# Performance work log

Measured on AMD Instinct MI355X. Metric: run time of the kernel, lower is better.

The kernel has to match this reference:

```python
import jax, jax.numpy as jnp
import numpy as np

BETA = 1.0
ALPHA = 0.5


def setup_inputs() -> dict:
    key = jax.random.key(0)
    k1, k2, k3 = jax.random.split(key, 3)
    B, N1, N2 = 512, 256, 32768
    v = jax.random.normal(k1, (B, N1), dtype=jnp.float32)
    mask = jax.random.uniform(k2, (B, N1), dtype=jnp.float32)
    Mem = jax.random.normal(k3, (N2, N1), dtype=jnp.float32)  # kernel [N2, N1] (trailing 1 squeezed)
    return {"v": v, "mask": mask, "Mem": Mem}


def reference(v, mask, Mem):
    # Squared L2 distance d2[i, b] = ||Mem[i] - v[b]||^2, computed without the
    # [N2, N1, B] diff tensor via the expansion ||m||^2 - 2 m.v + ||v||^2.
    m2 = jnp.sum(Mem * Mem, axis=1)            # [N2]
    v2 = jnp.sum(v * v, axis=1)                # [B]
    cross = jnp.einsum('nd,bd->nb', Mem, v)    # [N2, B]
    d2 = m2[:, None] - 2.0 * cross + v2[None, :]
    # Gaussian-kernel weights over the N2 stored patterns (softmax == exp/sum).
    w = jax.nn.softmax(-0.5 * BETA * d2, axis=0)  # [N2, B]
    # update[b] = sum_i w[i,b] * (Mem[i] - v[b]) = (w^T Mem)[b] - v[b]
    update = jnp.einsum('nb,nd->bd', w, Mem) - v   # [B, N1]
    return v + ALPHA * update * mask
```

## Files before the change

### kernel.cpp

```cpp
#include <hip/hip_runtime.h>
#include <hip/hip_bf16.h>
#include <stdint.h>

typedef float  f32x4  __attribute__((ext_vector_type(4)));
typedef float  f32x16 __attribute__((ext_vector_type(16)));
typedef _Float16 half8 __attribute__((ext_vector_type(8)));
typedef unsigned int uint32;

#define N1 256
#define N2T 32768
#define BQ 512
#define KT 32
#define TILE_B 16384

#define RA_OFF 0
#define MT_OFF 32768
#define LDS_BYTES 65536

union H4 { _Float16 h[4]; unsigned short s[4]; uint2 u2; };

#define GLD_LDS(gp, lp) __builtin_amdgcn_global_load_lds( \
    (const __attribute__((address_space(1))) void*)(gp), \
    (__attribute__((address_space(3))) void*)(lp), 16, 0, 0)

__global__ __launch_bounds__(256) void mhn_prep_k(
    const float* __restrict__ Mem, _Float16* __restrict__ MemA,
    _Float16* __restrict__ MemT, float* __restrict__ m2g)
{
  const int t   = blockIdx.x;
  const int tid = threadIdx.x;
  const int a    = tid >> 4;
  const int dblk = tid & 15;
  const int r0i  = 32*t + 2*a;

  const float* p0 = Mem + (size_t)r0i*N1 + dblk*16;
  const float* p1 = p0 + N1;
  float4 x0[4], x1[4];
  #pragma unroll
  for (int i=0;i<4;i++){ x0[i] = *(const float4*)(p0+4*i); x1[i] = *(const float4*)(p1+4*i); }

  float s0=0.f, s1=0.f;
  H4 h0[4], h1[4];
  #pragma unroll
  for (int i=0;i<4;i++){
    s0 += x0[i].x*x0[i].x + x0[i].y*x0[i].y + x0[i].z*x0[i].z + x0[i].w*x0[i].w;
    s1 += x1[i].x*x1[i].x + x1[i].y*x1[i].y + x1[i].z*x1[i].z + x1[i].w*x1[i].w;
    h0[i].h[0]=(_Float16)x0[i].x; h0[i].h[1]=(_Float16)x0[i].y; h0[i].h[2]=(_Float16)x0[i].z; h0[i].h[3]=(_Float16)x0[i].w;
    h1[i].h[0]=(_Float16)x1[i].x; h1[i].h[1]=(_Float16)x1[i].y; h1[i].h[2]=(_Float16)x1[i].z; h1[i].h[3]=(_Float16)x1[i].w;
  }

  char* bA = (char*)MemA + (size_t)t*TILE_B;
  {
    const int e0 = (2*a)&7, e1 = (2*a+1)&7;
    uint4 wv;
    wv.x=h0[0].u2.x; wv.y=h0[0].u2.y; wv.z=h0[1].u2.x; wv.w=h0[1].u2.y;
    *(uint4*)(bA + (2*a)*512   + (((2*dblk  )^e0)<<4)) = wv;
    wv.x=h0[2].u2.x; wv.y=h0[2].u2.y; wv.z=h0[3].u2.x; wv.w=h0[3].u2.y;
    *(uint4*)(bA + (2*a)*512   + (((2*dblk+1)^e0)<<4)) = wv;
    wv.x=h1[0].u2.x; wv.y=h1[0].u2.y; wv.z=h1[1].u2.x; wv.w=h1[1].u2.y;
    *(uint4*)(bA + (2*a+1)*512 + (((2*dblk  )^e1)<<4)) = wv;
    wv.x=h1[2].u2.x; wv.y=h1[2].u2.y; wv.z=h1[3].u2.x; wv.w=h1[3].u2.y;
    *(uint4*)(bA + (2*a+1)*512 + (((2*dblk+1)^e1)<<4)) = wv;
  }

  char* bT = (char*)MemT + (size_t)t*TILE_B;
  #pragma unroll
  for (int i=0;i<4;i++){
    #pragma unroll
    for (int j=0;j<4;j++){
      const int d = dblk*16 + 4*i + j;
      const uint32 pk = (uint32)h0[i].s[j] | ((uint32)h1[i].s[j] << 16);
      *(uint32*)(bT + d*64 + ((((a>>2) ^ ((d>>1)&3)))<<4) + ((a&3)<<2)) = pk;
    }
  }

  s0 += __shfl_xor(s0,1); s0 += __shfl_xor(s0,2); s0 += __shfl_xor(s0,4); s0 += __shfl_xor(s0,8);
  s1 += __shfl_xor(s1,1); s1 += __shfl_xor(s1,2); s1 += __shfl_xor(s1,4); s1 += __shfl_xor(s1,8);
  if (dblk == 0){ m2g[r0i] = -0.5f*s0; m2g[r0i+1] = -0.5f*s1; }
}

__global__ __launch_bounds__(256, 2) void mhn_flash_k(
    const _Float16* __restrict__ MemA, const _Float16* __restrict__ MemT,
    const float* __restrict__ m2g, const float* __restrict__ v,
    __hip_bfloat16* __restrict__ Opart, float* __restrict__ mpart,
    float* __restrict__ lpart, int CK, int nt)
{
  __shared__ __align__(16) char lds[LDS_BYTES];

  const int tid = threadIdx.x;
  const int w   = tid >> 6;
  const int l   = tid & 63;
  const int row = l & 31;
  const int hi  = l >> 5;

  const int nwg = gridDim.x;
  const int bid = blockIdx.x;
  const int s_  = (bid & 7) * (nwg >> 3) + (bid >> 3);
  const int c   = s_ >> 2;
  const int qb  = s_ & 3;

  const uint32 dmaL = (uint32)(w*4096 + l*16);
  const char* gA = (const char*)MemA + (size_t)(c*(CK>>5))*TILE_B + dmaL;
  const char* gT = (const char*)MemT + (size_t)(c*(CK>>5))*TILE_B + dmaL;
  char* const dA0 = lds + RA_OFF + dmaL;
  char* const dT0 = lds + MT_OFF + dmaL;

  #pragma unroll
  for (int i=0;i<4;i++){
    GLD_LDS(gA + i*1024, dA0 + i*1024);
    GLD_LDS(gT + i*1024, dT0 + i*1024);
  }
  gA += TILE_B; gT += TILE_B;

  half8 v8[16];
  const int q0 = qb*128 + w*32;
  {
    const float* vp = v + (size_t)(q0 + row)*N1 + 8*hi;
    #pragma unroll
    for (int s=0;s<16;s++){
      const float4 a = *(const float4*)(vp + 16*s);
      const float4 b = *(const float4*)(vp + 16*s + 4);
      half8 hv;
      hv[0]=(_Float16)a.x; hv[1]=(_Float16)a.y; hv[2]=(_Float16)a.z; hv[3]=(_Float16)a.w;
      hv[4]=(_Float16)b.x; hv[5]=(_Float16)b.y; hv[6]=(_Float16)b.z; hv[7]=(_Float16)b.w;
      v8[s]=hv;
    }
  }

  float mrun = -INFINITY, lrun = 0.f;
  f32x16 oacc[8];
  #pragma unroll
  for (int b=0;b<8;b++) oacc[b] = (f32x16)(0.f);

  const int e7 = row & 7;
  const uint32 qkB = (uint32)(row*512 + ((hi ^ (e7 & 1)) << 4) + ((e7 >> 1) << 5));
  const int sd = (row >> 1) & 3;
  const uint32 pvB = (uint32)(row*64 + ((hi ^ (sd & 1)) << 4) + ((sd >> 1) << 5));

  const float* m2p = m2g + c*CK + 8*0 + 4*hi;

  __syncthreads();

  for (int tt=0; tt<nt; ++tt){
    const uint32 bufO = (uint32)(tt & 1)*TILE_B;
    const bool pf = (tt+1 < nt);
    if (pf){
      const char* sA = gA; const char* sT = gT;
      char* dA = dA0 + (bufO ^ TILE_B);
      char* dT = dT0 + (bufO ^ TILE_B);
      #pragma unroll
      for (int i=0;i<4;i++){
        GLD_LDS(sA + i*1024, dA + i*1024);
        GLD_LDS(sT + i*1024, dT + i*1024);
      }
      gA += TILE_B; gT += TILE_B;
    }

    f32x4 m2v[4];
    #pragma unroll
    for (int b=0;b<4;b++) m2v[b] = *(const f32x4*)(m2p + 8*b);

    const char* ra = lds + RA_OFF + bufO;
    f32x16 S = (f32x16)(0.f);
    __builtin_amdgcn_s_setprio(1);
    #pragma unroll
    for (int s=0;s<16;s++){
      const half8 a = *(const half8*)(ra + (qkB ^ (uint32)(s<<5)));
      S = __builtin_amdgcn_mfma_f32_32x32x16_f16(a, v8[s], S, 0,0,0);
    }
    __builtin_amdgcn_s_setprio(0);

    float p[16];
    #pragma unroll
    for (int r=0;r<16;r++) p[r] = S[r] + m2v[r>>2][r&3];

    float t01=fmaxf(p[0],p[1]),   t23=fmaxf(p[2],p[3]),   t45=fmaxf(p[4],p[5]),   t67=fmaxf(p[6],p[7]);
    float t89=fmaxf(p[8],p[9]),   tAB=fmaxf(p[10],p[11]), tCD=fmaxf(p[12],p[13]), tEF=fmaxf(p[14],p[15]);
    float q03=fmaxf(t01,t23), q47=fmaxf(t45,t67), q8B=fmaxf(t89,tAB), qCF=fmaxf(tCD,tEF);
    float tm = fmaxf(fmaxf(q03,q47), fmaxf(q8B,qCF));
    tm = fmaxf(tm, __shfl_xor(tm, 32));
    if (__any(tm > mrun + 8.0f)){
      const float nm = fmaxf(mrun, tm);
      const float sc = __expf(mrun - nm);
      lrun *= sc; mrun = nm;
      #pragma unroll
      for (int b=0;b<8;b++) oacc[b] *= sc;
    }
    #pragma unroll
    for (int r=0;r<16;r++) p[r] = __expf(p[r] - mrun);

    uint32 D[8];
    #pragma unroll
    for (int i=0;i<8;i++){
      union { __fp16 h2 __attribute__((ext_vector_type(2))); uint32 u; } cv;
      cv.h2 = __builtin_amdgcn_cvt_pkrtz(p[2*i], p[2*i+1]);
      D[i] = cv.u;
    }
    uint32 wq[8];
    {
      const uint32 tD0 = (uint32)__shfl_xor((int)D[0], 32);
      const uint32 tD1 = (uint32)__shfl_xor((int)D[1], 32);
      const uint32 tD2 = (uint32)__shfl_xor((int)D[2], 32);
      const uint32 tD3 = (uint32)__shfl_xor((int)D[3], 32);
      const uint32 tD4 = (uint32)__shfl_xor((int)D[4], 32);
      const uint32 tD5 = (uint32)__shfl_xor((int)D[5], 32);
      const uint32 tD6 = (uint32)__shfl_xor((int)D[6], 32);
      const uint32 tD7 = (uint32)__shfl_xor((int)D[7], 32);
      const bool lo = (hi == 0);
      wq[0] = lo ? D[0] : tD2;  wq[1] = lo ? D[1] : tD3;
      wq[2] = lo ? tD0 : D[2];  wq[3] = lo ? tD1 : D[3];
      wq[4] = lo ? D[4] : tD6;  wq[5] = lo ? D[5] : tD7;
      wq[6] = lo ? tD4 : D[6];  wq[7] = lo ? tD5 : D[7];
    }
    union { uint32 u[4]; half8 h; } pb1, pb2;
    pb1.u[0]=wq[0]; pb1.u[1]=wq[1]; pb1.u[2]=wq[2]; pb1.u[3]=wq[3];
    pb2.u[0]=wq[4]; pb2.u[1]=wq[5]; pb2.u[2]=wq[6]; pb2.u[3]=wq[7];

    const char* mtb = lds + MT_OFF + bufO;
    const char* a1 = (const char*)(mtb + pvB);
    const char* a2 = (const char*)(mtb + (pvB ^ 32u));
    __builtin_amdgcn_s_setprio(1);
    #pragma unroll
    for (int b=0;b<8;b++){
      const half8 A1 = *(const half8*)(a1 + b*2048);
      oacc[b] = __builtin_amdgcn_mfma_f32_32x32x16_f16(A1, pb1.h, oacc[b], 0,0,0);
      const half8 A2 = *(const half8*)(a2 + b*2048);
      oacc[b] = __builtin_amdgcn_mfma_f32_32x32x16_f16(A2, pb2.h, oacc[b], 0,0,0);
    }
    __builtin_amdgcn_s_setprio(0);

    float s01=p[0]+p[1],   s23=p[2]+p[3],   s45=p[4]+p[5],   s67=p[6]+p[7];
    float s89=p[8]+p[9],   sAB=p[10]+p[11], sCD=p[12]+p[13], sEF=p[14]+p[15];
    float u03=s01+s23, u47=s45+s67, u8B=s89+sAB, uCF=sCD+sEF;
    float ps = (u03+u47) + (u8B+uCF);
    ps += __shfl_xor(ps, 32); lrun += ps;

    m2p += KT;
    __syncthreads();
  }

  {
    __hip_bfloat16* Op = Opart + (size_t)c*N1*BQ + (q0 + row);
    #pragma unroll
    for (int b=0;b<8;b++){
      #pragma unroll
      for (int r=0;r<16;r++){
        const int d = 32*b + (r&3) + 8*(r>>2) + 4*hi;
        Op[(size_t)d*BQ] = __float2bfloat16(oacc[b][r]);
      }
    }
    if (hi == 0){
      mpart[(size_t)c*BQ + q0 + row] = mrun;
      lpart[(size_t)c*BQ + q0 + row] = lrun;
    }
  }
}

__global__ __launch_bounds__(128) void mhn_wprep_k(
    const float* __restrict__ mpart, const float* __restrict__ lpart,
    float* __restrict__ W, float* __restrict__ invL, int nchunk)
{
  __shared__ float sred[2];
  const int q = blockIdx.x;
  const int c = threadIdx.x;
  const int l = c & 63, wv = c >> 6;

  const float m = (c < nchunk) ? mpart[(size_t)c*BQ + q] : -INFINITY;
  const float lv = (c < nchunk) ? lpart[(size_t)c*BQ + q] : 0.f;

  float r = m;
  r = fmaxf(r, __shfl_xor(r,1));  r = fmaxf(r, __shfl_xor(r,2));
  r = fmaxf(r, __shfl_xor(r,4));  r = fmaxf(r, __shfl_xor(r,8));
  r = fmaxf(r, __shfl_xor(r,16)); r = fmaxf(r, __shfl_xor(r,32));
  if (l == 0) sred[wv] = r;
  __syncthreads();
  const float M = fmaxf(sred[0], sred[1]);
  __syncthreads();

  const float e = __expf(m - M);
  float s = lv * e;
  s += __shfl_xor(s,1);  s += __shfl_xor(s,2);
  s += __shfl_xor(s,4);  s += __shfl_xor(s,8);
  s += __shfl_xor(s,16); s += __shfl_xor(s,32);
  if (l == 0) sred[wv] = s;
  __syncthreads();

  if (c < nchunk) W[(size_t)c*BQ + q] = e;
  if (c == 0) invL[q] = 1.0f / (sred[0] + sred[1]);
}

__global__ __launch_bounds__(256) void mhn_wsum_k(
    const float* __restrict__ v, const float* __restrict__ mask,
    const __hip_bfloat16* __restrict__ Opart, const float* __restrict__ W,
    const float* __restrict__ invL, float* __restrict__ out, int nchunk)
{
  const int g = blockIdx.x*256 + threadIdx.x;
  const int q = g & (BQ-1);
  const int d = g >> 9;

  const __hip_bfloat16* op = Opart + (size_t)d*BQ + q;
  const float* wp = W + q;
  float acc = 0.f;
  #pragma unroll 8
  for (int c2=0; c2<nchunk; c2++){
    acc += __bfloat162float(op[(size_t)c2*N1*BQ]) * wp[(size_t)c2*BQ];
  }
  const float vv = v[(size_t)q*N1 + d], mk = mask[(size_t)q*N1 + d];
  out[(size_t)q*N1 + d] = vv + 0.5f*(acc*invL[q] - vv)*mk;
}

extern "C" void kernel_launch(void* const* d_in, const int* in_sizes, int n_in,
                              void* d_out, int out_size, void* d_ws, size_t ws_size,
                              hipStream_t stream)
{
  (void)in_sizes; (void)n_in; (void)out_size;
  const float* v    = (const float*)d_in[0];
  const float* mask = (const float*)d_in[1];
  const float* Mem  = (const float*)d_in[2];
  float* out = (float*)d_out;

  const size_t fixedB   = (size_t)N2T*N1*2*2 + (size_t)N2T*4 + (size_t)BQ*4;
  const size_t perChunk = (size_t)BQ*N1*2 + (size_t)BQ*12;
  int nchunk = 128;
  while (nchunk > 4 && fixedB + (size_t)nchunk*perChunk > ws_size) nchunk >>= 1;

  char* wsb = (char*)d_ws;
  _Float16* MemA = (_Float16*)wsb;
  _Float16* MemT = (_Float16*)(wsb + (size_t)N2T*N1*2);
  float*    m2g  = (float*)(wsb + (size_t)N2T*N1*4);
  float*    invL = (float*)(wsb + (size_t)N2T*N1*4 + (size_t)N2T*4);
  char* pb = wsb + fixedB;
  __hip_bfloat16* Opart = (__hip_bfloat16*)pb;
  float* mpart = (float*)(pb + (size_t)nchunk*BQ*N1*2);
  float* lpart = mpart + (size_t)nchunk*BQ;
  float* W     = lpart + (size_t)nchunk*BQ;

  const int CK = N2T / nchunk;
  const int nt = CK / KT;

  mhn_prep_k<<<dim3(N2T/KT), dim3(256), 0, stream>>>(Mem, MemA, MemT, m2g);
  mhn_flash_k<<<dim3(4*nchunk), dim3(256), 0, stream>>>(MemA, MemT, m2g, v, Opart, mpart, lpart, CK, nt);
  mhn_wprep_k<<<dim3(BQ), dim3(128), 0, stream>>>(mpart, lpart, W, invL, nchunk);
  mhn_wsum_k<<<dim3((N1*BQ)/256), dim3(256), 0, stream>>>(v, mask, Opart, W, invL, out, nchunk);
}
```

Measured before the change: 69.40 us.

## Fuse softmax combine kernels and prefetch LDS operands in flash MFMA loops

Merges the weight-prep and weighted-sum kernels into one combine kernel. Each block recomputes the per-query max and normaliser for 64 queries, keeps the chunk weights in shared memory and writes coalesced output through an LDS transpose. This removes one launch and the W/invL round trip through global memory. In the flash kernel, LDS A-operand reads for both MFMA loops are software-prefetched into registers ahead of use to hide LDS latency, at the cost of extra VGPRs. The combine kernel redundantly rereads mpart/lpart in every d-block.

```diff
diff --git a/kernel.cpp b/kernel.cpp
--- a/kernel.cpp
+++ b/kernel.cpp
@@ -137,7 +137,7 @@
   const int sd = (row >> 1) & 3;
   const uint32 pvB = (uint32)(row*64 + ((hi ^ (sd & 1)) << 4) + ((sd >> 1) << 5));
 
-  const float* m2p = m2g + c*CK + 8*0 + 4*hi;
+  const float* m2p = m2g + c*CK + 4*hi;
 
   __syncthreads();
 
@@ -161,11 +161,15 @@
     for (int b=0;b<4;b++) m2v[b] = *(const f32x4*)(m2p + 8*b);
 
     const char* ra = lds + RA_OFF + bufO;
+    half8 aq[4];
+    #pragma unroll
+    for (int i=0;i<4;i++) aq[i] = *(const half8*)(ra + (qkB ^ (uint32)(i<<5)));
     f32x16 S = (f32x16)(0.f);
     __builtin_amdgcn_s_setprio(1);
     #pragma unroll
     for (int s=0;s<16;s++){
-      const half8 a = *(const half8*)(ra + (qkB ^ (uint32)(s<<5)));
+      const half8 a = aq[s&3];
+      if (s < 12) aq[s&3] = *(const half8*)(ra + (qkB ^ (uint32)((s+4)<<5)));
       S = __builtin_amdgcn_mfma_f32_32x32x16_f16(a, v8[s], S, 0,0,0);
     }
     __builtin_amdgcn_s_setprio(0);
@@ -219,12 +223,19 @@
     const char* mtb = lds + MT_OFF + bufO;
     const char* a1 = (const char*)(mtb + pvB);
     const char* a2 = (const char*)(mtb + (pvB ^ 32u));
+    half8 r1[2], r2[2];
+    r1[0] = *(const half8*)(a1);
+    r2[0] = *(const half8*)(a2);
     __builtin_amdgcn_s_setprio(1);
     #pragma unroll
     for (int b=0;b<8;b++){
-      const half8 A1 = *(const half8*)(a1 + b*2048);
+      const half8 A1 = r1[b&1];
+      const half8 A2 = r2[b&1];
+      if (b < 7){
+        r1[(b+1)&1] = *(const half8*)(a1 + (b+1)*2048);
+        r2[(b+1)&1] = *(const half8*)(a2 + (b+1)*2048);
+      }
       oacc[b] = __builtin_amdgcn_mfma_f32_32x32x16_f16(A1, pb1.h, oacc[b], 0,0,0);
-      const half8 A2 = *(const half8*)(a2 + b*2048);
       oacc[b] = __builtin_amdgcn_mfma_f32_32x32x16_f16(A2, pb2.h, oacc[b], 0,0,0);
     }
     __builtin_amdgcn_s_setprio(0);
@@ -256,57 +267,58 @@
   }
 }
 
-__global__ __launch_bounds__(128) void mhn_wprep_k(
-    const float* __restrict__ mpart, const float* __restrict__ lpart,
-    float* __restrict__ W, float* __restrict__ invL, int nchunk)
+__global__ __launch_bounds__(256) void mhn_combine_k(
+    const float* __restrict__ v, const float* __restrict__ mask,
+    const __hip_bfloat16* __restrict__ Opart, const float* __restrict__ mpart,
+    const float* __restrict__ lpart, float* __restrict__ out, int nchunk)
 {
-  __shared__ float sred[2];
-  const int q = blockIdx.x;
-  const int c = threadIdx.x;
-  const int l = c & 63, wv = c >> 6;
-
-  const float m = (c < nchunk) ? mpart[(size_t)c*BQ + q] : -INFINITY;
-  const float lv = (c < nchunk) ? lpart[(size_t)c*BQ + q] : 0.f;
-
-  float r = m;
-  r = fmaxf(r, __shfl_xor(r,1));  r = fmaxf(r, __shfl_xor(r,2));
-  r = fmaxf(r, __shfl_xor(r,4));  r = fmaxf(r, __shfl_xor(r,8));
-  r = fmaxf(r, __shfl_xor(r,16)); r = fmaxf(r, __shfl_xor(r,32));
-  if (l == 0) sred[wv] = r;
-  __syncthreads();
-  const float M = fmaxf(sred[0], sred[1]);
-  __syncthreads();
-
-  const float e = __expf(m - M);
-  float s = lv * e;
-  s += __shfl_xor(s,1);  s += __shfl_xor(s,2);
-  s += __shfl_xor(s,4);  s += __shfl_xor(s,8);
-  s += __shfl_xor(s,16); s += __shfl_xor(s,32);
-  if (l == 0) sred[wv] = s;
-  __syncthreads();
-
-  if (c < nchunk) W[(size_t)c*BQ + q] = e;
-  if (c == 0) invL[q] = 1.0f / (sred[0] + sred[1]);
-}
-
-__global__ __launch_bounds__(256) void mhn_wsum_k(
-    const float* __restrict__ v, const float* __restrict__ mask,
-    const __hip_bfloat16* __restrict__ Opart, const float* __restrict__ W,
-    const float* __restrict__ invL, float* __restrict__ out, int nchunk)
-{
-  const int g = blockIdx.x*256 + threadIdx.x;
-  const int q = g & (BQ-1);
-  const int d = g >> 9;
-
-  const __hip_bfloat16* op = Opart + (size_t)d*BQ + q;
-  const float* wp = W + q;
+  __shared__ float Wl[128][64];
+  __shared__ float red[4][64];
+  __shared__ float Mq[64];
+  __shared__ float iLq[64];
+  __shared__ float T[256];
+
+  const int bid = blockIdx.x;
+  const int q0  = (bid & 7) * 64;
+  const int d0  = (bid >> 3) * 4;
+  const int t   = threadIdx.x;
+  const int q   = t & 63;
+  const int cg  = t >> 6;
+  const int nc4 = nchunk >> 2;
+
+  float mx = -INFINITY;
+  for (int k=0;k<nc4;k++)
+    mx = fmaxf(mx, mpart[(size_t)(cg*nc4+k)*BQ + q0 + q]);
+  red[cg][q] = mx;
+  __syncthreads();
+  if (t < 64) Mq[t] = fmaxf(fmaxf(red[0][t],red[1][t]), fmaxf(red[2][t],red[3][t]));
+  __syncthreads();
+  const float M = Mq[q];
+  float ls = 0.f;
+  for (int k=0;k<nc4;k++){
+    const int cc = cg*nc4 + k;
+    const float e = __expf(mpart[(size_t)cc*BQ + q0 + q] - M);
+    Wl[cc][q] = e;
+    ls += lpart[(size_t)cc*BQ + q0 + q] * e;
+  }
+  red[cg][q] = ls;
+  __syncthreads();
+  if (t < 64) iLq[t] = 1.0f / (((red[0][t]+red[1][t]) + (red[2][t]+red[3][t])));
+  __syncthreads();
+
+  const int dl = t >> 6;
+  const __hip_bfloat16* op = Opart + (size_t)(d0+dl)*BQ + q0 + q;
   float acc = 0.f;
   #pragma unroll 8
-  for (int c2=0; c2<nchunk; c2++){
-    acc += __bfloat162float(op[(size_t)c2*N1*BQ]) * wp[(size_t)c2*BQ];
-  }
-  const float vv = v[(size_t)q*N1 + d], mk = mask[(size_t)q*N1 + d];
-  out[(size_t)q*N1 + d] = vv + 0.5f*(acc*invL[q] - vv)*mk;
+  for (int c2=0; c2<nchunk; c2++)
+    acc += __bfloat162float(op[(size_t)c2*N1*BQ]) * Wl[c2][q];
+  T[q*4 + dl] = acc * iLq[q];
+  __syncthreads();
+
+  const int q2 = t >> 2, d2 = t & 3;
+  const size_t oi = (size_t)(q0+q2)*N1 + d0 + d2;
+  const float vv = v[oi], mk = mask[oi];
+  out[oi] = vv + 0.5f*(T[t] - vv)*mk;
 }
 
 extern "C" void kernel_launch(void* const* d_in, const int* in_sizes, int n_in,
@@ -319,8 +331,8 @@
   const float* Mem  = (const float*)d_in[2];
   float* out = (float*)d_out;
 
-  const size_t fixedB   = (size_t)N2T*N1*2*2 + (size_t)N2T*4 + (size_t)BQ*4;
-  const size_t perChunk = (size_t)BQ*N1*2 + (size_t)BQ*12;
+  const size_t fixedB   = (size_t)N2T*N1*2*2 + (size_t)N2T*4;
+  const size_t perChunk = (size_t)BQ*N1*2 + (size_t)BQ*8;
   int nchunk = 128;
   while (nchunk > 4 && fixedB + (size_t)nchunk*perChunk > ws_size) nchunk >>= 1;
 
@@ -328,18 +340,15 @@
   _Float16* MemA = (_Float16*)wsb;
   _Float16* MemT = (_Float16*)(wsb + (size_t)N2T*N1*2);
   float*    m2g  = (float*)(wsb + (size_t)N2T*N1*4);
-  float*    invL = (float*)(wsb + (size_t)N2T*N1*4 + (size_t)N2T*4);
   char* pb = wsb + fixedB;
   __hip_bfloat16* Opart = (__hip_bfloat16*)pb;
   float* mpart = (float*)(pb + (size_t)nchunk*BQ*N1*2);
   float* lpart = mpart + (size_t)nchunk*BQ;
-  float* W     = lpart + (size_t)nchunk*BQ;
 
   const int CK = N2T / nchunk;
   const int nt = CK / KT;
 
   mhn_prep_k<<<dim3(N2T/KT), dim3(256), 0, stream>>>(Mem, MemA, MemT, m2g);
   mhn_flash_k<<<dim3(4*nchunk), dim3(256), 0, stream>>>(MemA, MemT, m2g, v, Opart, mpart, lpart, CK, nt);
-  mhn_wprep_k<<<dim3(BQ), dim3(128), 0, stream>>>(mpart, lpart, W, invL, nchunk);
-  mhn_wsum_k<<<dim3((N1*BQ)/256), dim3(256), 0, stream>>>(v, mask, Opart, W, invL, out, nchunk);
+  mhn_combine_k<<<dim3(512), dim3(256), 0, stream>>>(v, mask, Opart, mpart, lpart, out, nchunk);
 }
```

Measured after the change: 73.41 us. 1.06x slower.

## Process two query tiles per wave to reuse each LDS Mem fragment twice

Applied to the files above, without the earlier changes.

Each wave now handles 64 queries as two 32-query sub-tiles, so every half8 fragment read from LDS feeds two MFMAs in both the score and the accumulation GEMMs. The grid halves, so each workgroup covers 256 queries and the global/LDS traffic for Mem tiles is amortised over twice the queries. The cost is doubled accumulator and v-fragment registers, which forces launch bounds down to one block per SIMD-group. The setprio hints are also dropped. Lower occupancy and fewer workgroups may hurt latency hiding.

```diff
diff --git a/kernel.cpp b/kernel.cpp
--- a/kernel.cpp
+++ b/kernel.cpp
@@ -79,7 +79,7 @@
   if (dblk == 0){ m2g[r0i] = -0.5f*s0; m2g[r0i+1] = -0.5f*s1; }
 }
 
-__global__ __launch_bounds__(256, 2) void mhn_flash_k(
+__global__ __launch_bounds__(256, 1) void mhn_flash_k(
     const _Float16* __restrict__ MemA, const _Float16* __restrict__ MemT,
     const float* __restrict__ m2g, const float* __restrict__ v,
     __hip_bfloat16* __restrict__ Opart, float* __restrict__ mpart,
@@ -96,8 +96,8 @@
   const int nwg = gridDim.x;
   const int bid = blockIdx.x;
   const int s_  = (bid & 7) * (nwg >> 3) + (bid >> 3);
-  const int c   = s_ >> 2;
-  const int qb  = s_ & 3;
+  const int c   = s_ >> 1;
+  const int qh  = s_ & 1;
 
   const uint32 dmaL = (uint32)(w*4096 + l*16);
   const char* gA = (const char*)MemA + (size_t)(c*(CK>>5))*TILE_B + dmaL;
@@ -112,32 +112,38 @@
   }
   gA += TILE_B; gT += TILE_B;
 
-  half8 v8[16];
-  const int q0 = qb*128 + w*32;
+  half8 v8a[16], v8b[16];
+  const int q0 = qh*256 + w*64;
   {
-    const float* vp = v + (size_t)(q0 + row)*N1 + 8*hi;
+    const float* vpa = v + (size_t)(q0 + row)*N1 + 8*hi;
+    const float* vpb = vpa + 32*N1;
     #pragma unroll
     for (int s=0;s<16;s++){
-      const float4 a = *(const float4*)(vp + 16*s);
-      const float4 b = *(const float4*)(vp + 16*s + 4);
+      float4 a = *(const float4*)(vpa + 16*s);
+      float4 b = *(const float4*)(vpa + 16*s + 4);
       half8 hv;
       hv[0]=(_Float16)a.x; hv[1]=(_Float16)a.y; hv[2]=(_Float16)a.z; hv[3]=(_Float16)a.w;
       hv[4]=(_Float16)b.x; hv[5]=(_Float16)b.y; hv[6]=(_Float16)b.z; hv[7]=(_Float16)b.w;
-      v8[s]=hv;
-    }
-  }
-
-  float mrun = -INFINITY, lrun = 0.f;
-  f32x16 oacc[8];
-  #pragma unroll
-  for (int b=0;b<8;b++) oacc[b] = (f32x16)(0.f);
+      v8a[s]=hv;
+      a = *(const float4*)(vpb + 16*s);
+      b = *(const float4*)(vpb + 16*s + 4);
+      hv[0]=(_Float16)a.x; hv[1]=(_Float16)a.y; hv[2]=(_Float16)a.z; hv[3]=(_Float16)a.w;
+      hv[4]=(_Float16)b.x; hv[5]=(_Float16)b.y; hv[6]=(_Float16)b.z; hv[7]=(_Float16)b.w;
+      v8b[s]=hv;
+    }
+  }
+
+  float mrun0=-INFINITY, mrun1=-INFINITY, lrun0=0.f, lrun1=0.f;
+  f32x16 oA[8], oB[8];
+  #pragma unroll
+  for (int b=0;b<8;b++){ oA[b]=(f32x16)(0.f); oB[b]=(f32x16)(0.f); }
 
   const int e7 = row & 7;
   const uint32 qkB = (uint32)(row*512 + ((hi ^ (e7 & 1)) << 4) + ((e7 >> 1) << 5));
   const int sd = (row >> 1) & 3;
   const uint32 pvB = (uint32)(row*64 + ((hi ^ (sd & 1)) << 4) + ((sd >> 1) << 5));
 
-  const float* m2p = m2g + c*CK + 8*0 + 4*hi;
+  const float* m2p = m2g + c*CK + 4*hi;
 
   __syncthreads();
 
@@ -161,79 +167,82 @@
     for (int b=0;b<4;b++) m2v[b] = *(const f32x4*)(m2p + 8*b);
 
     const char* ra = lds + RA_OFF + bufO;
-    f32x16 S = (f32x16)(0.f);
-    __builtin_amdgcn_s_setprio(1);
+    f32x16 S0 = (f32x16)(0.f), S1 = (f32x16)(0.f);
     #pragma unroll
     for (int s=0;s<16;s++){
       const half8 a = *(const half8*)(ra + (qkB ^ (uint32)(s<<5)));
-      S = __builtin_amdgcn_mfma_f32_32x32x16_f16(a, v8[s], S, 0,0,0);
-    }
-    __builtin_amdgcn_s_setprio(0);
-
-    float p[16];
-    #pragma unroll
-    for (int r=0;r<16;r++) p[r] = S[r] + m2v[r>>2][r&3];
-
-    float t01=fmaxf(p[0],p[1]),   t23=fmaxf(p[2],p[3]),   t45=fmaxf(p[4],p[5]),   t67=fmaxf(p[6],p[7]);
-    float t89=fmaxf(p[8],p[9]),   tAB=fmaxf(p[10],p[11]), tCD=fmaxf(p[12],p[13]), tEF=fmaxf(p[14],p[15]);
-    float q03=fmaxf(t01,t23), q47=fmaxf(t45,t67), q8B=fmaxf(t89,tAB), qCF=fmaxf(tCD,tEF);
-    float tm = fmaxf(fmaxf(q03,q47), fmaxf(q8B,qCF));
-    tm = fmaxf(tm, __shfl_xor(tm, 32));
-    if (__any(tm > mrun + 8.0f)){
-      const float nm = fmaxf(mrun, tm);
-      const float sc = __expf(mrun - nm);
-      lrun *= sc; mrun = nm;
+      S0 = __builtin_amdgcn_mfma_f32_32x32x16_f16(a, v8a[s], S0, 0,0,0);
+      S1 = __builtin_amdgcn_mfma_f32_32x32x16_f16(a, v8b[s], S1, 0,0,0);
+    }
+
+    float p0[16], p1[16];
+    #pragma unroll
+    for (int r=0;r<16;r++){ p0[r] = S0[r] + m2v[r>>2][r&3]; p1[r] = S1[r] + m2v[r>>2][r&3]; }
+
+    float tm0 = p0[0], tm1 = p1[0];
+    #pragma unroll
+    for (int r=1;r<16;r++){ tm0 = fmaxf(tm0, p0[r]); tm1 = fmaxf(tm1, p1[r]); }
+    tm0 = fmaxf(tm0, __shfl_xor(tm0, 32));
+    tm1 = fmaxf(tm1, __shfl_xor(tm1, 32));
+    if (__any((tm0 > mrun0 + 8.0f) || (tm1 > mrun1 + 8.0f))){
+      const float nm0 = fmaxf(mrun0, tm0), nm1 = fmaxf(mrun1, tm1);
+      const float sc0 = __expf(mrun0 - nm0), sc1 = __expf(mrun1 - nm1);
+      lrun0 *= sc0; mrun0 = nm0;
+      lrun1 *= sc1; mrun1 = nm1;
       #pragma unroll
-      for (int b=0;b<8;b++) oacc[b] *= sc;
-    }
-    #pragma unroll
-    for (int r=0;r<16;r++) p[r] = __expf(p[r] - mrun);
-
-    uint32 D[8];
+      for (int b=0;b<8;b++){ oA[b] *= sc0; oB[b] *= sc1; }
+    }
+    #pragma unroll
+    for (int r=0;r<16;r++){ p0[r] = __expf(p0[r] - mrun0); p1[r] = __expf(p1[r] - mrun1); }
+
+    uint32 D0[8], D1[8];
     #pragma unroll
     for (int i=0;i<8;i++){
       union { __fp16 h2 __attribute__((ext_vector_type(2))); uint32 u; } cv;
-      cv.h2 = __builtin_amdgcn_cvt_pkrtz(p[2*i], p[2*i+1]);
-      D[i] = cv.u;
-    }
-    uint32 wq[8];
+      cv.h2 = __builtin_amdgcn_cvt_pkrtz(p0[2*i], p0[2*i+1]); D0[i] = cv.u;
+      cv.h2 = __builtin_amdgcn_cvt_pkrtz(p1[2*i], p1[2*i+1]); D1[i] = cv.u;
+    }
+    const bool lo = (hi == 0);
+    union { uint32 u[4]; half8 h; } pb1a, pb2a, pb1b, pb2b;
     {
-      const uint32 tD0 = (uint32)__shfl_xor((int)D[0], 32);
-      const uint32 tD1 = (uint32)__shfl_xor((int)D[1], 32);
-      const uint32 tD2 = (uint32)__shfl_xor((int)D[2], 32);
-      const uint32 tD3 = (uint32)__shfl_xor((int)D[3], 32);
-      const uint32 tD4 = (uint32)__shfl_xor((int)D[4], 32);
-      const uint32 tD5 = (uint32)__shfl_xor((int)D[5], 32);
-      const uint32 tD6 = (uint32)__shfl_xor((int)D[6], 32);
-      const uint32 tD7 = (uint32)__shfl_xor((int)D[7], 32);
-      const bool lo = (hi == 0);
-      wq[0] = lo ? D[0] : tD2;  wq[1] = lo ? D[1] : tD3;
-      wq[2] = lo ? tD0 : D[2];  wq[3] = lo ? tD1 : D[3];
-      wq[4] = lo ? D[4] : tD6;  wq[5] = lo ? D[5] : tD7;
-      wq[6] = lo ? tD4 : D[6];  wq[7] = lo ? tD5 : D[7];
-    }
-    union { uint32 u[4]; half8 h; } pb1, pb2;
-    pb1.u[0]=wq[0]; pb1.u[1]=wq[1]; pb1.u[2]=wq[2]; pb1.u[3]=wq[3];
-    pb2.u[0]=wq[4]; pb2.u[1]=wq[5]; pb2.u[2]=wq[6]; pb2.u[3]=wq[7];
+      const uint32 t0=(uint32)__shfl_xor((int)D0[0],32), t1=(uint32)__shfl_xor((int)D0[1],32);
+      const uint32 t2=(uint32)__shfl_xor((int)D0[2],32), t3=(uint32)__shfl_xor((int)D0[3],32);
+      const uint32 t4=(uint32)__shfl_xor((int)D0[4],32), t5=(uint32)__shfl_xor((int)D0[5],32);
+      const uint32 t6=(uint32)__shfl_xor((int)D0[6],32), t7=(uint32)__shfl_xor((int)D0[7],32);
+      pb1a.u[0]= lo?D0[0]:t2;  pb1a.u[1]= lo?D0[1]:t3;
+      pb1a.u[2]= lo?t0:D0[2];  pb1a.u[3]= lo?t1:D0[3];
+      pb2a.u[0]= lo?D0[4]:t6;  pb2a.u[1]= lo?D0[5]:t7;
+      pb2a.u[2]= lo?t4:D0[6];  pb2a.u[3]= lo?t5:D0[7];
+    }
+    {
+      const uint32 t0=(uint32)__shfl_xor((int)D1[0],32), t1=(uint32)__shfl_xor((int)D1[1],32);
+      const uint32 t2=(uint32)__shfl_xor((int)D1[2],32), t3=(uint32)__shfl_xor((int)D1[3],32);
+      const uint32 t4=(uint32)__shfl_xor((int)D1[4],32), t5=(uint32)__shfl_xor((int)D1[5],32);
+      const uint32 t6=(uint32)__shfl_xor((int)D1[6],32), t7=(uint32)__shfl_xor((int)D1[7],32);
+      pb1b.u[0]= lo?D1[0]:t2;  pb1b.u[1]= lo?D1[1]:t3;
+      pb1b.u[2]= lo?t0:D1[2];  pb1b.u[3]= lo?t1:D1[3];
+      pb2b.u[0]= lo?D1[4]:t6;  pb2b.u[1]= lo?D1[5]:t7;
+      pb2b.u[2]= lo?t4:D1[6];  pb2b.u[3]= lo?t5:D1[7];
+    }
 
     const char* mtb = lds + MT_OFF + bufO;
     const char* a1 = (const char*)(mtb + pvB);
     const char* a2 = (const char*)(mtb + (pvB ^ 32u));
-    __builtin_amdgcn_s_setprio(1);
     #pragma unroll
     for (int b=0;b<8;b++){
       const half8 A1 = *(const half8*)(a1 + b*2048);
-      oacc[b] = __builtin_amdgcn_mfma_f32_32x32x16_f16(A1, pb1.h, oacc[b], 0,0,0);
+      oA[b] = __builtin_amdgcn_mfma_f32_32x32x16_f16(A1, pb1a.h, oA[b], 0,0,0);
+      oB[b] = __builtin_amdgcn_mfma_f32_32x32x16_f16(A1, pb1b.h, oB[b], 0,0,0);
       const half8 A2 = *(const half8*)(a2 + b*2048);
-      oacc[b] = __builtin_amdgcn_mfma_f32_32x32x16_f16(A2, pb2.h, oacc[b], 0,0,0);
-    }
-    __builtin_amdgcn_s_setprio(0);
-
-    float s01=p[0]+p[1],   s23=p[2]+p[3],   s45=p[4]+p[5],   s67=p[6]+p[7];
-    float s89=p[8]+p[9],   sAB=p[10]+p[11], sCD=p[12]+p[13], sEF=p[14]+p[15];
-    float u03=s01+s23, u47=s45+s67, u8B=s89+sAB, uCF=sCD+sEF;
-    float ps = (u03+u47) + (u8B+uCF);
-    ps += __shfl_xor(ps, 32); lrun += ps;
+      oA[b] = __builtin_amdgcn_mfma_f32_32x32x16_f16(A2, pb2a.h, oA[b], 0,0,0);
+      oB[b] = __builtin_amdgcn_mfma_f32_32x32x16_f16(A2, pb2b.h, oB[b], 0,0,0);
+    }
+
+    float ps0 = 0.f, ps1 = 0.f;
+    #pragma unroll
+    for (int r=0;r<16;r++){ ps0 += p0[r]; ps1 += p1[r]; }
+    ps0 += __shfl_xor(ps0, 32); lrun0 += ps0;
+    ps1 += __shfl_xor(ps1, 32); lrun1 += ps1;
 
     m2p += KT;
     __syncthreads();
@@ -246,12 +255,15 @@
       #pragma unroll
       for (int r=0;r<16;r++){
         const int d = 32*b + (r&3) + 8*(r>>2) + 4*hi;
-        Op[(size_t)d*BQ] = __float2bfloat16(oacc[b][r]);
+        Op[(size_t)d*BQ]      = __float2bfloat16(oA[b][r]);
+        Op[(size_t)d*BQ + 32] = __float2bfloat16(oB[b][r]);
       }
     }
     if (hi == 0){
-      mpart[(size_t)c*BQ + q0 + row] = mrun;
-      lpart[(size_t)c*BQ + q0 + row] = lrun;
+      mpart[(size_t)c*BQ + q0 + row]      = mrun0;
+      lpart[(size_t)c*BQ + q0 + row]      = lrun0;
+      mpart[(size_t)c*BQ + q0 + 32 + row] = mrun1;
+      lpart[(size_t)c*BQ + q0 + 32 + row] = lrun1;
     }
   }
 }
@@ -339,7 +351,7 @@
   const int nt = CK / KT;
 
   mhn_prep_k<<<dim3(N2T/KT), dim3(256), 0, stream>>>(Mem, MemA, MemT, m2g);
-  mhn_flash_k<<<dim3(4*nchunk), dim3(256), 0, stream>>>(MemA, MemT, m2g, v, Opart, mpart, lpart, CK, nt);
+  mhn_flash_k<<<dim3(2*nchunk), dim3(256), 0, stream>>>(MemA, MemT, m2g, v, Opart, mpart, lpart, CK, nt);
   mhn_wprep_k<<<dim3(BQ), dim3(128), 0, stream>>>(mpart, lpart, W, invL, nchunk);
   mhn_wsum_k<<<dim3((N1*BQ)/256), dim3(256), 0, stream>>>(v, mask, Opart, W, invL, out, nchunk);
 }
```

Result: slower. 202.3 us (+191.5%).
